# Optimization experiments

Hardware: AMD Instinct MI355X
Metric: run time of the kernel (lower is better)

The kernel has to match this reference:

```python
import jax, jax.numpy as jnp
import numpy as np

HEADS = 16
DIM_HEAD = 64
ROT_DIM = 32  # RotaryEmbedding(dim=dim_head//2) -> rotates first 32 channels
SCALE = DIM_HEAD ** -0.5


def _rope(x):
    # x: [b, h, n, d]; rotate first ROT_DIM channels, interleaved pairs (lucidrains style)
    n = x.shape[2]
    inv_freq = 1.0 / (10000.0 ** (jnp.arange(0, ROT_DIM, 2, dtype=jnp.float32) / ROT_DIM))  # [16]
    ang = jnp.arange(n, dtype=jnp.float32)[:, None] * inv_freq[None, :]  # [n, 16]
    cos, sin = jnp.cos(ang), jnp.sin(ang)  # [n, 16]
    x_rot, x_pass = x[..., :ROT_DIM], x[..., ROT_DIM:]
    x1 = x_rot[..., 0::2]  # [b,h,n,16]
    x2 = x_rot[..., 1::2]
    y1 = x1 * cos - x2 * sin
    y2 = x2 * cos + x1 * sin
    y = jnp.stack([y1, y2], axis=-1).reshape(x_rot.shape)  # re-interleave
    return jnp.concatenate([y, x_pass], axis=-1)


def setup_inputs() -> dict:
    key = jax.random.key(0)
    ks = jax.random.split(key, 5)
    b, n, d = 4, 2048, 1024
    inner = HEADS * DIM_HEAD
    return {
        "queries": jax.random.normal(ks[0], (b, n, d), jnp.float32),
        "Wq": jax.random.normal(ks[1], (d, inner), jnp.float32) * (d ** -0.5),
        "Wkv": jax.random.normal(ks[2], (d, 2 * inner), jnp.float32) * (d ** -0.5),
        "Wout": jax.random.normal(ks[3], (inner, d), jnp.float32) * (inner ** -0.5),
        "bout": jnp.zeros((d,), jnp.float32),
    }


def reference(queries, Wq, Wkv, Wout, bout):
    b, n, _ = queries.shape
    q = queries @ Wq                      # [b,n,inner]
    kv = queries @ Wkv                    # self-attention: context = queries
    k, v = jnp.split(kv, 2, axis=-1)
    split_heads = lambda t: t.reshape(b, n, HEADS, DIM_HEAD).transpose(0, 2, 1, 3)
    q, k, v = split_heads(q), split_heads(k), split_heads(v)
    q, k = _rope(q), _rope(k)
    sim = jnp.einsum('bhid,bhjd->bhij', q, k) * SCALE
    attn = jax.nn.softmax(sim, axis=-1)
    out = jnp.einsum('bhij,bhjd->bhid', attn, v)
    out = out.transpose(0, 2, 1, 3).reshape(b, n, HEADS * DIM_HEAD)
    return out @ Wout + bout
```

## Files before the change

### kernel.cpp

```cpp
#include <hip/hip_runtime.h>
#include <math.h>

#define BB    4
#define NN    2048
#define DD    1024
#define HH    16
#define DHD   64
#define INNER 1024
#define LOG2_10K_D16 0.8304820237218406f
#define SCALE_LOG2E 0.1803368801111601f

typedef short bf16x8 __attribute__((ext_vector_type(8)));
typedef short bf16x4 __attribute__((ext_vector_type(4)));
typedef float f32x4  __attribute__((ext_vector_type(4)));
typedef unsigned short u16x8 __attribute__((ext_vector_type(8)));

#define ASYNC16(g, l) __builtin_amdgcn_global_load_lds( \
    (const __attribute__((address_space(1))) void*)(g),  \
    (__attribute__((address_space(3))) void*)(l), 16, 0, 0)

#define MFMA16(a, b, c) __builtin_amdgcn_mfma_f32_16x16x32_bf16((a), (b), (c), 0, 0, 0)

static __device__ __forceinline__ float fexp2(float x) {
#if __has_builtin(__builtin_amdgcn_exp2f)
    return __builtin_amdgcn_exp2f(x);
#else
    float r;
    asm("v_exp_f32 %0, %1" : "=v"(r) : "v"(x));
    return r;
#endif
}

static __device__ __forceinline__ unsigned short f2bf(float f) {
    union { float f; unsigned int u; } v; v.f = f;
    unsigned int u = v.u;
    u += 0x7fffu + ((u >> 16) & 1u);
    return (unsigned short)(u >> 16);
}
static __device__ __forceinline__ unsigned int packbf2(float lo, float hi) {
    union { float f; unsigned int u; } a, b;
    a.f = lo; b.f = hi;
    return __builtin_amdgcn_perm(b.u + 0x8000u, a.u + 0x8000u, 0x07060302u);
}

__global__ __launch_bounds__(256) void cast_x_kernel(
    const float* __restrict__ X, unsigned short* __restrict__ Xb)
{
    const size_t i = ((size_t)blockIdx.x * 256 + threadIdx.x) * 8;
    const float4 a = *(const float4*)(X + i);
    const float4 b = *(const float4*)(X + i + 4);
    u16x8 o;
    o[0] = f2bf(a.x); o[1] = f2bf(a.y); o[2] = f2bf(a.z); o[3] = f2bf(a.w);
    o[4] = f2bf(b.x); o[5] = f2bf(b.y); o[6] = f2bf(b.z); o[7] = f2bf(b.w);
    *(u16x8*)(Xb + i) = o;
}

__global__ __launch_bounds__(256) void tcast_kernel(
    const float* __restrict__ src, unsigned short* __restrict__ dst,
    int K, int N)
{
    __shared__ float ts[32][33];
    const int t = threadIdx.x;
    const int n0 = blockIdx.x * 32, k0 = blockIdx.y * 32;
    const int r = t >> 5, c = t & 31;
    #pragma unroll
    for (int p = 0; p < 4; ++p)
        ts[r + p * 8][c] = src[(size_t)(k0 + r + p * 8) * N + n0 + c];
    __syncthreads();
    #pragma unroll
    for (int p = 0; p < 4; ++p)
        dst[(size_t)(n0 + r + p * 8) * K + k0 + c] = f2bf(ts[c][r + p * 8]);
}

__global__ __launch_bounds__(256) void proj_qkv_mfma(
    const unsigned short* __restrict__ Xb, const unsigned short* __restrict__ Wt,
    unsigned short* __restrict__ qb, unsigned short* __restrict__ kb,
    unsigned short* __restrict__ vb)
{
    __shared__ __align__(16) unsigned short As[128 * 32];
    __shared__ __align__(16) unsigned short Bs[128 * 32];

    const int t     = threadIdx.x;
    const int w     = t >> 6, lane = t & 63;
    const int lane4 = lane & 15, quad = lane >> 4, quad8 = quad * 8;
    const int wm    = w >> 1, wn = w & 1;
    const int m0    = blockIdx.y * 128, n0 = blockIdx.x * 128;

    const int srow = t >> 2, scol = (t & 3) * 8;
    const unsigned short* gA = Xb + (size_t)(m0 + srow) * DD + scol;
    const unsigned short* gB = Wt + (size_t)(n0 + srow) * DD + scol;
    unsigned short* lA = As + t * 8;
    unsigned short* lB = Bs + t * 8;

    f32x4 acc[4][4] = {};

    for (int k0 = 0; k0 < DD; k0 += 32) {
        __syncthreads();
        ASYNC16(gA + k0,            lA);
        ASYNC16(gA + 64 * DD + k0,  lA + 2048);
        ASYNC16(gB + k0,            lB);
        ASYNC16(gB + 64 * DD + k0,  lB + 2048);
        __syncthreads();

        bf16x8 a[4], b[4];
        #pragma unroll
        for (int i = 0; i < 4; ++i)
            a[i] = *(const bf16x8*)&As[(wm * 64 + i * 16 + lane4) * 32 + quad8];
        #pragma unroll
        for (int j = 0; j < 4; ++j)
            b[j] = *(const bf16x8*)&Bs[(wn * 64 + j * 16 + lane4) * 32 + quad8];
        #pragma unroll
        for (int i = 0; i < 4; ++i)
            #pragma unroll
            for (int j = 0; j < 4; ++j)
                acc[i][j] = MFMA16(a[i], b[j], acc[i][j]);
    }

    const int sec = n0 >> 10;

    if (sec == 2) {
        #pragma unroll
        for (int j = 0; j < 4; ++j) {
            const int csec = (n0 & 1023) + wn * 64 + j * 16;
            const int h    = csec >> 6;
            const int dh   = (csec & 63) + lane4;
            #pragma unroll
            for (int i = 0; i < 4; ++i) {
                const int rg0 = m0 + wm * 64 + i * 16 + quad * 4;
                const int b   = rg0 >> 11;
                const int n   = rg0 & 2047;
                uint2 pk;
                pk.x = packbf2(acc[i][j][0], acc[i][j][1]);
                pk.y = packbf2(acc[i][j][2], acc[i][j][3]);
                *(uint2*)(vb + (((size_t)b * HH + h) * DHD + dh) * NN + n) = pk;
            }
        }
    } else {
        unsigned short* dst = (sec == 0) ? qb : kb;
        const float qscale = (sec == 0) ? SCALE_LOG2E : 1.0f;
        #pragma unroll
        for (int j = 0; j < 4; ++j) {
            const int csec = (n0 & 1023) + wn * 64 + j * 16;
            const int h    = csec >> 6;
            const int dhb  = csec & 63;
            const int dh   = dhb + lane4;
            const bool rope = (dhb < 32);
            const float invf = fexp2(-(float)(dh >> 1) * LOG2_10K_D16);
            #pragma unroll
            for (int i = 0; i < 4; ++i) {
                #pragma unroll
                for (int r = 0; r < 4; ++r) {
                    const int rg = m0 + wm * 64 + i * 16 + quad * 4 + r;
                    const int b  = rg >> 11;
                    const int n  = rg & 2047;
                    float x = acc[i][j][r] * qscale;
                    if (rope) {
                        const float ang = (float)n * invf;
                        float s_, c_;
                        __sincosf(ang, &s_, &c_);
                        const float p = __shfl_xor(x, 1);
                        x = (lane4 & 1) ? fmaf(p, s_, x * c_)
                                        : fmaf(p, -s_, x * c_);
                    }
                    dst[(((size_t)b * HH + h) * NN + n) * DHD + dh] = f2bf(x);
                }
            }
        }
    }
}

__global__ __launch_bounds__(256, 2) void attn_kernel(
    const unsigned short* __restrict__ qb, const unsigned short* __restrict__ kb,
    const unsigned short* __restrict__ vtb, unsigned short* __restrict__ aob)
{
    __shared__ __align__(16) unsigned char smem[65536];
    unsigned short (*ks)[128][64] = (unsigned short (*)[128][64])smem;
    unsigned short (*vs)[64][128] = (unsigned short (*)[64][128])(smem + 32768);

    const int t     = threadIdx.x;
    const int kq    = t >> 6;
    const int lane  = t & 63;
    const int lane4 = lane & 15;
    const int quad  = lane >> 4;
    const int quad8 = quad * 8;
    const int l7    = lane4 & 7;

    const int bid = blockIdx.x;
    const int bh  = bid & 63;
    const int q0  = (bid >> 6) * 64;
    const size_t hb = (size_t)bh * NN * DHD;

    bf16x8 qf[4][2];
    #pragma unroll
    for (int qt = 0; qt < 4; ++qt) {
        const unsigned short* qrow = qb + hb + (size_t)(q0 + qt * 16 + lane4) * DHD;
        qf[qt][0] = *(const bf16x8*)(qrow + quad8);
        qf[qt][1] = *(const bf16x8*)(qrow + 32 + quad8);
    }

    bf16x8 onesf;
    #pragma unroll
    for (int j = 0; j < 8; ++j) onesf[j] = (short)0x3F80;

    const int krow0 = t >> 3;
    const int kcol  = ((t & 7) ^ (krow0 & 7)) * 8;
    const unsigned short* kg = kb + hb + (size_t)krow0 * DHD + (t & 7) * 8;
    const int vrow0 = t >> 4;
    const int vm    = t & 15;
    const int vr7   = vrow0 & 7;
    const int vcX   = (vm >> 1) & 3;
    const int vsub  = vm >> 3;
    const int vqA   = (2 * vm) & 3;
    const int vqB   = (2 * vm + 1) & 3;
    const int colA  = (((vcX * 4 + vqA) ^ vr7) * 8) + vsub * 4;
    const int colB  = (((vcX * 4 + vqB) ^ vr7) * 8) + vsub * 4;
    const unsigned short* vg = vtb + hb + (size_t)vrow0 * NN + vm * 8;

    f32x4 o[4][4], lacc[4];
    #pragma unroll
    for (int d = 0; d < 4; ++d)
        #pragma unroll
        for (int qt = 0; qt < 4; ++qt) o[d][qt] = (f32x4){0.f, 0.f, 0.f, 0.f};
    #pragma unroll
    for (int qt = 0; qt < 4; ++qt) lacc[qt] = (f32x4){0.f, 0.f, 0.f, 0.f};

    {
        bf16x8 kv[4], vv[4];
        #pragma unroll
        for (int s = 0; s < 4; ++s) {
            kv[s] = *(const bf16x8*)(kg + (size_t)s * 32 * DHD);
            vv[s] = *(const bf16x8*)(vg + (size_t)s * 16 * NN);
        }
        #pragma unroll
        for (int s = 0; s < 4; ++s) {
            *(bf16x8*)&ks[0][krow0 + 32 * s][kcol] = kv[s];
            bf16x4 lo = __builtin_shufflevector(vv[s], vv[s], 0, 1, 2, 3);
            bf16x4 hi = __builtin_shufflevector(vv[s], vv[s], 4, 5, 6, 7);
            *(bf16x4*)&vs[0][vrow0 + 16 * s][colA] = lo;
            *(bf16x4*)&vs[0][vrow0 + 16 * s][colB] = hi;
        }
    }
    __syncthreads();

    for (int kt = 0; kt < NN / 128; ++kt) {
        const int cur = kt & 1;
        const bool more = (kt + 1 < NN / 128);

        bf16x8 kv[4], vv[4];
        if (more) {
            #pragma unroll
            for (int s = 0; s < 4; ++s) {
                kv[s] = *(const bf16x8*)(kg + (size_t)(kt + 1) * 128 * DHD + (size_t)s * 32 * DHD);
                vv[s] = *(const bf16x8*)(vg + (kt + 1) * 128 + (size_t)s * 16 * NN);
            }
        }

        bf16x8 ak[2][2];
        #pragma unroll
        for (int sub = 0; sub < 2; ++sub) {
            const int row = sub * 64 + kq * 16 + lane4;
            ak[sub][0] = *(const bf16x8*)&ks[cur][row][(quad ^ l7) * 8];
            ak[sub][1] = *(const bf16x8*)&ks[cur][row][((quad + 4) ^ l7) * 8];
        }

        bf16x8 pb[4];
        #pragma unroll
        for (int qt = 0; qt < 4; ++qt) {
            f32x4 z0 = (f32x4){0.f, 0.f, 0.f, 0.f};
            f32x4 z1 = (f32x4){0.f, 0.f, 0.f, 0.f};
            z0 = MFMA16(ak[0][0], qf[qt][0], z0);
            z0 = MFMA16(ak[0][1], qf[qt][1], z0);
            z1 = MFMA16(ak[1][0], qf[qt][0], z1);
            z1 = MFMA16(ak[1][1], qf[qt][1], z1);
            union { unsigned int u[4]; bf16x8 v; } pk;
            pk.u[0] = packbf2(fexp2(z0[0]), fexp2(z0[1]));
            pk.u[1] = packbf2(fexp2(z0[2]), fexp2(z0[3]));
            pk.u[2] = packbf2(fexp2(z1[0]), fexp2(z1[1]));
            pk.u[3] = packbf2(fexp2(z1[2]), fexp2(z1[3]));
            pb[qt] = pk.v;
            lacc[qt] = MFMA16(onesf, pb[qt], lacc[qt]);
        }

        #pragma unroll
        for (int d = 0; d < 4; ++d) {
            const bf16x8 av = *(const bf16x8*)&vs[cur][d * 16 + lane4][((kq * 4 + quad) ^ l7) * 8];
            #pragma unroll
            for (int qt = 0; qt < 4; ++qt)
                o[d][qt] = MFMA16(av, pb[qt], o[d][qt]);
        }

        if (more) {
            #pragma unroll
            for (int s = 0; s < 4; ++s) {
                *(bf16x8*)&ks[cur ^ 1][krow0 + 32 * s][kcol] = kv[s];
                bf16x4 lo = __builtin_shufflevector(vv[s], vv[s], 0, 1, 2, 3);
                bf16x4 hi = __builtin_shufflevector(vv[s], vv[s], 4, 5, 6, 7);
                *(bf16x4*)&vs[cur ^ 1][vrow0 + 16 * s][colA] = lo;
                *(bf16x4*)&vs[cur ^ 1][vrow0 + 16 * s][colB] = hi;
            }
        }
        __syncthreads();
    }

    float* pbuf = (float*)smem;
    #pragma unroll
    for (int d = 0; d < 4; ++d)
        #pragma unroll
        for (int qt = 0; qt < 4; ++qt)
            #pragma unroll
            for (int r = 0; r < 4; ++r)
                pbuf[(kq * 64 + d * 16 + quad * 4 + r) * 64 + qt * 16 + lane4] = o[d][qt][r];
    __syncthreads();

    f32x4 of[4];
    #pragma unroll
    for (int d = 0; d < 4; ++d)
        #pragma unroll
        for (int r = 0; r < 4; ++r) {
            const int dh = d * 16 + quad * 4 + r;
            const int qc = kq * 16 + lane4;
            of[d][r] = pbuf[dh * 64 + qc] + pbuf[(64 + dh) * 64 + qc]
                     + pbuf[(128 + dh) * 64 + qc] + pbuf[(192 + dh) * 64 + qc];
        }
    __syncthreads();

    if (quad == 0) {
        #pragma unroll
        for (int qt = 0; qt < 4; ++qt)
            pbuf[(kq * 4 + qt) * 16 + lane4] = lacc[qt][0];
    }
    __syncthreads();
    const float lt = pbuf[(0 * 4 + kq) * 16 + lane4] + pbuf[(1 * 4 + kq) * 16 + lane4]
                   + pbuf[(2 * 4 + kq) * 16 + lane4] + pbuf[(3 * 4 + kq) * 16 + lane4];
    const float linv = 1.0f / lt;

    const int b = bh >> 4, h = bh & 15;
    const int n = q0 + kq * 16 + lane4;
    unsigned short* obase = aob + ((size_t)b * NN + n) * INNER + h * DHD;
    #pragma unroll
    for (int d = 0; d < 4; ++d) {
        uint2 pk;
        pk.x = packbf2(of[d][0] * linv, of[d][1] * linv);
        pk.y = packbf2(of[d][2] * linv, of[d][3] * linv);
        *(uint2*)(obase + d * 16 + quad * 4) = pk;
    }
}

__global__ __launch_bounds__(256) void out_proj_mfma(
    const unsigned short* __restrict__ Ab, const unsigned short* __restrict__ Wt,
    const float* __restrict__ bias, float* __restrict__ C)
{
    __shared__ __align__(16) unsigned short As[128 * 32];
    __shared__ __align__(16) unsigned short Bs[128 * 32];

    const int t     = threadIdx.x;
    const int w     = t >> 6, lane = t & 63;
    const int lane4 = lane & 15, quad = lane >> 4, quad8 = quad * 8;
    const int wm    = w >> 1, wn = w & 1;
    const int m0    = blockIdx.y * 128, n0 = blockIdx.x * 128;

    const int srow = t >> 2, scol = (t & 3) * 8;
    const unsigned short* gA = Ab + (size_t)(m0 + srow) * INNER + scol;
    const unsigned short* gB = Wt + (size_t)(n0 + srow) * INNER + scol;
    unsigned short* lA = As + t * 8;
    unsigned short* lB = Bs + t * 8;

    f32x4 acc[4][4] = {};

    for (int k0 = 0; k0 < INNER; k0 += 32) {
        __syncthreads();
        ASYNC16(gA + k0,               lA);
        ASYNC16(gA + 64 * INNER + k0,  lA + 2048);
        ASYNC16(gB + k0,               lB);
        ASYNC16(gB + 64 * INNER + k0,  lB + 2048);
        __syncthreads();

        bf16x8 a[4], b[4];
        #pragma unroll
        for (int i = 0; i < 4; ++i)
            a[i] = *(const bf16x8*)&As[(wm * 64 + i * 16 + lane4) * 32 + quad8];
        #pragma unroll
        for (int j = 0; j < 4; ++j)
            b[j] = *(const bf16x8*)&Bs[(wn * 64 + j * 16 + lane4) * 32 + quad8];
        #pragma unroll
        for (int i = 0; i < 4; ++i)
            #pragma unroll
            for (int j = 0; j < 4; ++j)
                acc[i][j] = MFMA16(a[i], b[j], acc[i][j]);
    }

    #pragma unroll
    for (int j = 0; j < 4; ++j) {
        const int col = n0 + wn * 64 + j * 16 + lane4;
        const float bv = bias[col];
        #pragma unroll
        for (int i = 0; i < 4; ++i)
            #pragma unroll
            for (int r = 0; r < 4; ++r) {
                const int rg = m0 + wm * 64 + i * 16 + quad * 4 + r;
                C[(size_t)rg * DD + col] = acc[i][j][r] + bv;
            }
    }
}

extern "C" void kernel_launch(void* const* d_in, const int* in_sizes, int n_in,
                              void* d_out, int out_size, void* d_ws, size_t ws_size,
                              hipStream_t stream)
{
    const float* X    = (const float*)d_in[0];
    const float* Wq   = (const float*)d_in[1];
    const float* Wkv  = (const float*)d_in[2];
    const float* Wout = (const float*)d_in[3];
    const float* bout = (const float*)d_in[4];
    float* out = (float*)d_out;

    const size_t E = (size_t)BB * HH * NN * DHD;
    unsigned short* qb  = (unsigned short*)d_ws;
    unsigned short* kb  = qb + E;
    unsigned short* vtb = kb + E;
    unsigned short* xb  = vtb + E;
    unsigned short* wt  = xb + E;
    unsigned short* wo  = wt + (size_t)3072 * 1024;

    cast_x_kernel<<<4096, 256, 0, stream>>>(X, xb);
    tcast_kernel<<<dim3(32, 32), 256, 0, stream>>>(Wq,   wt,               1024, 1024);
    tcast_kernel<<<dim3(64, 32), 256, 0, stream>>>(Wkv,  wt + 1024 * 1024, 1024, 2048);
    tcast_kernel<<<dim3(32, 32), 256, 0, stream>>>(Wout, wo,               1024, 1024);

    proj_qkv_mfma<<<dim3(3072 / 128, 8192 / 128), 256, 0, stream>>>(
        xb, wt, qb, kb, vtb);

    attn_kernel<<<dim3(NN / 64 * BB * HH), 256, 0, stream>>>(qb, kb, vtb, xb);

    out_proj_mfma<<<dim3(1024 / 128, 8192 / 128), 256, 0, stream>>>(
        xb, wo, bout, out);
}
```

Before: 299.2 us.

## Make K/V LDS tiles wave-private and drop per-iteration block barriers

Remaps the global-to-LDS loading of K and V so each wave writes exactly the K rows and V column slices it later reads for its own kq slice. With no cross-wave sharing of the staged tiles, the per-iteration __syncthreads in the key loop is removed, and only one barrier is kept before the shared reduction buffer is reused. The aim is to let waves drift independently and overlap memory and MFMA work instead of stalling at a barrier every tile. The risk is a correctness hazard if any LDS element is read by a wave other than the one that wrote it, and the changed access pattern may alter global coalescing or LDS bank conflicts.

```diff
diff --git a/kernel.cpp b/kernel.cpp
--- a/kernel.cpp
+++ b/kernel.cpp
@@ -202,18 +202,16 @@
     #pragma unroll
     for (int j = 0; j < 8; ++j) onesf[j] = (short)0x3F80;
 
-    const int krow0 = t >> 3;
-    const int kcol  = ((t & 7) ^ (krow0 & 7)) * 8;
-    const unsigned short* kg = kb + hb + (size_t)krow0 * DHD + (t & 7) * 8;
-    const int vrow0 = t >> 4;
-    const int vm    = t & 15;
+    const int krow  = kq * 16 + (lane >> 3);
+    const int kslot = ((lane & 7) ^ (lane >> 3)) * 8;
+    const unsigned short* kg = kb + hb + (size_t)krow * DHD + (lane & 7) * 8;
+
+    const int vrow0 = lane >> 2;
+    const int vm    = 2 * kq + (lane & 1) + ((lane >> 1) & 1) * 8;
     const int vr7   = vrow0 & 7;
-    const int vcX   = (vm >> 1) & 3;
-    const int vsub  = vm >> 3;
-    const int vqA   = (2 * vm) & 3;
-    const int vqB   = (2 * vm + 1) & 3;
-    const int colA  = (((vcX * 4 + vqA) ^ vr7) * 8) + vsub * 4;
-    const int colB  = (((vcX * 4 + vqB) ^ vr7) * 8) + vsub * 4;
+    const int halfo = (vm >> 3) * 4;
+    const int colA  = ((((vm & 7) * 2)     ^ vr7) * 8) + halfo;
+    const int colB  = ((((vm & 7) * 2 + 1) ^ vr7) * 8) + halfo;
     const unsigned short* vg = vtb + hb + (size_t)vrow0 * NN + vm * 8;
 
     f32x4 o[4][4], lacc[4];
@@ -225,34 +223,44 @@
     for (int qt = 0; qt < 4; ++qt) lacc[qt] = (f32x4){0.f, 0.f, 0.f, 0.f};
 
     {
-        bf16x8 kv[4], vv[4];
+        const bf16x8 k0 = *(const bf16x8*)(kg);
+        const bf16x8 k1 = *(const bf16x8*)(kg + 8 * DHD);
+        const bf16x8 k2 = *(const bf16x8*)(kg + 64 * DHD);
+        const bf16x8 k3 = *(const bf16x8*)(kg + 72 * DHD);
+        const bf16x8 v0 = *(const bf16x8*)(vg);
+        const bf16x8 v1 = *(const bf16x8*)(vg + (size_t)16 * NN);
+        const bf16x8 v2 = *(const bf16x8*)(vg + (size_t)32 * NN);
+        const bf16x8 v3 = *(const bf16x8*)(vg + (size_t)48 * NN);
+        *(bf16x8*)&ks[0][krow][kslot]      = k0;
+        *(bf16x8*)&ks[0][krow + 8][kslot]  = k1;
+        *(bf16x8*)&ks[0][krow + 64][kslot] = k2;
+        *(bf16x8*)&ks[0][krow + 72][kslot] = k3;
         #pragma unroll
         for (int s = 0; s < 4; ++s) {
-            kv[s] = *(const bf16x8*)(kg + (size_t)s * 32 * DHD);
-            vv[s] = *(const bf16x8*)(vg + (size_t)s * 16 * NN);
-        }
-        #pragma unroll
-        for (int s = 0; s < 4; ++s) {
-            *(bf16x8*)&ks[0][krow0 + 32 * s][kcol] = kv[s];
-            bf16x4 lo = __builtin_shufflevector(vv[s], vv[s], 0, 1, 2, 3);
-            bf16x4 hi = __builtin_shufflevector(vv[s], vv[s], 4, 5, 6, 7);
+            const bf16x8 vv = (s == 0) ? v0 : (s == 1) ? v1 : (s == 2) ? v2 : v3;
+            bf16x4 lo = __builtin_shufflevector(vv, vv, 0, 1, 2, 3);
+            bf16x4 hi = __builtin_shufflevector(vv, vv, 4, 5, 6, 7);
             *(bf16x4*)&vs[0][vrow0 + 16 * s][colA] = lo;
             *(bf16x4*)&vs[0][vrow0 + 16 * s][colB] = hi;
         }
     }
-    __syncthreads();
 
     for (int kt = 0; kt < NN / 128; ++kt) {
         const int cur = kt & 1;
         const bool more = (kt + 1 < NN / 128);
 
-        bf16x8 kv[4], vv[4];
+        bf16x8 nk0, nk1, nk2, nk3, nv0, nv1, nv2, nv3;
         if (more) {
-            #pragma unroll
-            for (int s = 0; s < 4; ++s) {
-                kv[s] = *(const bf16x8*)(kg + (size_t)(kt + 1) * 128 * DHD + (size_t)s * 32 * DHD);
-                vv[s] = *(const bf16x8*)(vg + (kt + 1) * 128 + (size_t)s * 16 * NN);
-            }
+            const unsigned short* kgn = kg + (size_t)(kt + 1) * 128 * DHD;
+            const unsigned short* vgn = vg + (kt + 1) * 128;
+            nk0 = *(const bf16x8*)(kgn);
+            nk1 = *(const bf16x8*)(kgn + 8 * DHD);
+            nk2 = *(const bf16x8*)(kgn + 64 * DHD);
+            nk3 = *(const bf16x8*)(kgn + 72 * DHD);
+            nv0 = *(const bf16x8*)(vgn);
+            nv1 = *(const bf16x8*)(vgn + (size_t)16 * NN);
+            nv2 = *(const bf16x8*)(vgn + (size_t)32 * NN);
+            nv3 = *(const bf16x8*)(vgn + (size_t)48 * NN);
         }
 
         bf16x8 ak[2][2];
@@ -290,18 +298,23 @@
         }
 
         if (more) {
+            const int nb = cur ^ 1;
+            *(bf16x8*)&ks[nb][krow][kslot]      = nk0;
+            *(bf16x8*)&ks[nb][krow + 8][kslot]  = nk1;
+            *(bf16x8*)&ks[nb][krow + 64][kslot] = nk2;
+            *(bf16x8*)&ks[nb][krow + 72][kslot] = nk3;
             #pragma unroll
             for (int s = 0; s < 4; ++s) {
-                *(bf16x8*)&ks[cur ^ 1][krow0 + 32 * s][kcol] = kv[s];
-                bf16x4 lo = __builtin_shufflevector(vv[s], vv[s], 0, 1, 2, 3);
-                bf16x4 hi = __builtin_shufflevector(vv[s], vv[s], 4, 5, 6, 7);
-                *(bf16x4*)&vs[cur ^ 1][vrow0 + 16 * s][colA] = lo;
-                *(bf16x4*)&vs[cur ^ 1][vrow0 + 16 * s][colB] = hi;
+                const bf16x8 vv = (s == 0) ? nv0 : (s == 1) ? nv1 : (s == 2) ? nv2 : nv3;
+                bf16x4 lo = __builtin_shufflevector(vv, vv, 0, 1, 2, 3);
+                bf16x4 hi = __builtin_shufflevector(vv, vv, 4, 5, 6, 7);
+                *(bf16x4*)&vs[nb][vrow0 + 16 * s][colA] = lo;
+                *(bf16x4*)&vs[nb][vrow0 + 16 * s][colB] = hi;
             }
         }
-        __syncthreads();
-    }
-
+    }
+
+    __syncthreads();
     float* pbuf = (float*)smem;
     #pragma unroll
     for (int d = 0; d < 4; ++d)
```

New measurement: 312.2 us. +4.4%, slower.

## Load K/V fragments directly from global into registers, drop LDS staging

Applied to the files above, without the earlier changes.

The attention kernel no longer stages K and V tiles through shared memory with barriers. Each wave now loads its own MFMA fragments straight from global memory into registers, double-buffered across two register sets. The row-sum is computed with scalar adds plus cross-lane shuffles instead of a ones-vector MFMA. This removes LDS writes and reads and the per-tile __syncthreads, but each wave now fetches its fragments on its own with narrower, less coalesced loads. It also raises register pressure under the 2-blocks-per-CU launch bound.

```diff
diff --git a/kernel.cpp b/kernel.cpp
--- a/kernel.cpp
+++ b/kernel.cpp
@@ -174,8 +174,6 @@
     const unsigned short* __restrict__ vtb, unsigned short* __restrict__ aob)
 {
     __shared__ __align__(16) unsigned char smem[65536];
-    unsigned short (*ks)[128][64] = (unsigned short (*)[128][64])smem;
-    unsigned short (*vs)[64][128] = (unsigned short (*)[64][128])(smem + 32768);
 
     const int t     = threadIdx.x;
     const int kq    = t >> 6;
@@ -183,7 +181,6 @@
     const int lane4 = lane & 15;
     const int quad  = lane >> 4;
     const int quad8 = quad * 8;
-    const int l7    = lane4 & 7;
 
     const int bid = blockIdx.x;
     const int bh  = bid & 63;
@@ -198,108 +195,91 @@
         qf[qt][1] = *(const bf16x8*)(qrow + 32 + quad8);
     }
 
-    bf16x8 onesf;
-    #pragma unroll
-    for (int j = 0; j < 8; ++j) onesf[j] = (short)0x3F80;
-
-    const int krow0 = t >> 3;
-    const int kcol  = ((t & 7) ^ (krow0 & 7)) * 8;
-    const unsigned short* kg = kb + hb + (size_t)krow0 * DHD + (t & 7) * 8;
-    const int vrow0 = t >> 4;
-    const int vm    = t & 15;
-    const int vr7   = vrow0 & 7;
-    const int vcX   = (vm >> 1) & 3;
-    const int vsub  = vm >> 3;
-    const int vqA   = (2 * vm) & 3;
-    const int vqB   = (2 * vm + 1) & 3;
-    const int colA  = (((vcX * 4 + vqA) ^ vr7) * 8) + vsub * 4;
-    const int colB  = (((vcX * 4 + vqB) ^ vr7) * 8) + vsub * 4;
-    const unsigned short* vg = vtb + hb + (size_t)vrow0 * NN + vm * 8;
-
-    f32x4 o[4][4], lacc[4];
+    const unsigned short* kfb = kb + hb + (size_t)(kq * 16 + lane4) * DHD + quad8;
+    const unsigned short* vflo = vtb + hb + (size_t)lane4 * NN + kq * 16 + quad * 4;
+    const unsigned short* vfhi = vflo + 64;
+
+    f32x4 o[4][4];
+    float lsum[4] = {0.f, 0.f, 0.f, 0.f};
     #pragma unroll
     for (int d = 0; d < 4; ++d)
         #pragma unroll
         for (int qt = 0; qt < 4; ++qt) o[d][qt] = (f32x4){0.f, 0.f, 0.f, 0.f};
-    #pragma unroll
-    for (int qt = 0; qt < 4; ++qt) lacc[qt] = (f32x4){0.f, 0.f, 0.f, 0.f};
-
-    {
-        bf16x8 kv[4], vv[4];
-        #pragma unroll
-        for (int s = 0; s < 4; ++s) {
-            kv[s] = *(const bf16x8*)(kg + (size_t)s * 32 * DHD);
-            vv[s] = *(const bf16x8*)(vg + (size_t)s * 16 * NN);
+
+    bf16x8 akA[2][2], akB[2][2];
+    bf16x4 avloA[4], avhiA[4], avloB[4], avhiB[4];
+
+#define LOADK(dst, kt) do {                                                      \
+    dst[0][0] = *(const bf16x8*)(kfb + (size_t)((kt) * 128)      * DHD);         \
+    dst[0][1] = *(const bf16x8*)(kfb + (size_t)((kt) * 128)      * DHD + 32);    \
+    dst[1][0] = *(const bf16x8*)(kfb + (size_t)((kt) * 128 + 64) * DHD);         \
+    dst[1][1] = *(const bf16x8*)(kfb + (size_t)((kt) * 128 + 64) * DHD + 32);    \
+} while (0)
+
+#define LOADV(dlo, dhi, kt) do {                                                 \
+    _Pragma("unroll")                                                            \
+    for (int d_ = 0; d_ < 4; ++d_) {                                             \
+        dlo[d_] = *(const bf16x4*)(vflo + (size_t)d_ * 16 * NN + (kt) * 128);    \
+        dhi[d_] = *(const bf16x4*)(vfhi + (size_t)d_ * 16 * NN + (kt) * 128);    \
+    }                                                                            \
+} while (0)
+
+#define COMPUTE(ak, avlo, avhi) do {                                             \
+    bf16x8 pb_[4];                                                               \
+    _Pragma("unroll")                                                            \
+    for (int qt_ = 0; qt_ < 4; ++qt_) {                                          \
+        f32x4 z0 = (f32x4){0.f, 0.f, 0.f, 0.f};                                  \
+        f32x4 z1 = (f32x4){0.f, 0.f, 0.f, 0.f};                                  \
+        z0 = MFMA16(ak[0][0], qf[qt_][0], z0);                                   \
+        z0 = MFMA16(ak[0][1], qf[qt_][1], z0);                                   \
+        z1 = MFMA16(ak[1][0], qf[qt_][0], z1);                                   \
+        z1 = MFMA16(ak[1][1], qf[qt_][1], z1);                                   \
+        const float e00 = fexp2(z0[0]), e01 = fexp2(z0[1]);                      \
+        const float e02 = fexp2(z0[2]), e03 = fexp2(z0[3]);                      \
+        const float e10 = fexp2(z1[0]), e11 = fexp2(z1[1]);                      \
+        const float e12 = fexp2(z1[2]), e13 = fexp2(z1[3]);                      \
+        union { unsigned int u[4]; bf16x8 v; } pk_;                              \
+        pk_.u[0] = packbf2(e00, e01);                                            \
+        pk_.u[1] = packbf2(e02, e03);                                            \
+        pk_.u[2] = packbf2(e10, e11);                                            \
+        pk_.u[3] = packbf2(e12, e13);                                            \
+        pb_[qt_] = pk_.v;                                                        \
+        lsum[qt_] += ((e00 + e01) + (e02 + e03)) + ((e10 + e11) + (e12 + e13));  \
+    }                                                                            \
+    _Pragma("unroll")                                                            \
+    for (int d_ = 0; d_ < 4; ++d_) {                                             \
+        const bf16x8 av_ = __builtin_shufflevector(avlo[d_], avhi[d_],           \
+                                                   0, 1, 2, 3, 4, 5, 6, 7);      \
+        _Pragma("unroll")                                                        \
+        for (int qt_ = 0; qt_ < 4; ++qt_)                                        \
+            o[d_][qt_] = MFMA16(av_, pb_[qt_], o[d_][qt_]);                      \
+    }                                                                            \
+} while (0)
+
+    LOADK(akA, 0);
+    LOADV(avloA, avhiA, 0);
+
+    for (int kt = 0; kt < NN / 128; kt += 2) {
+        LOADK(akB, kt + 1);
+        LOADV(avloB, avhiB, kt + 1);
+        COMPUTE(akA, avloA, avhiA);
+        if (kt + 2 < NN / 128) {
+            LOADK(akA, kt + 2);
+            LOADV(avloA, avhiA, kt + 2);
         }
-        #pragma unroll
-        for (int s = 0; s < 4; ++s) {
-            *(bf16x8*)&ks[0][krow0 + 32 * s][kcol] = kv[s];
-            bf16x4 lo = __builtin_shufflevector(vv[s], vv[s], 0, 1, 2, 3);
-            bf16x4 hi = __builtin_shufflevector(vv[s], vv[s], 4, 5, 6, 7);
-            *(bf16x4*)&vs[0][vrow0 + 16 * s][colA] = lo;
-            *(bf16x4*)&vs[0][vrow0 + 16 * s][colB] = hi;
-        }
-    }
-    __syncthreads();
-
-    for (int kt = 0; kt < NN / 128; ++kt) {
-        const int cur = kt & 1;
-        const bool more = (kt + 1 < NN / 128);
-
-        bf16x8 kv[4], vv[4];
-        if (more) {
-            #pragma unroll
-            for (int s = 0; s < 4; ++s) {
-                kv[s] = *(const bf16x8*)(kg + (size_t)(kt + 1) * 128 * DHD + (size_t)s * 32 * DHD);
-                vv[s] = *(const bf16x8*)(vg + (kt + 1) * 128 + (size_t)s * 16 * NN);
-            }
-        }
-
-        bf16x8 ak[2][2];
-        #pragma unroll
-        for (int sub = 0; sub < 2; ++sub) {
-            const int row = sub * 64 + kq * 16 + lane4;
-            ak[sub][0] = *(const bf16x8*)&ks[cur][row][(quad ^ l7) * 8];
-            ak[sub][1] = *(const bf16x8*)&ks[cur][row][((quad + 4) ^ l7) * 8];
-        }
-
-        bf16x8 pb[4];
-        #pragma unroll
-        for (int qt = 0; qt < 4; ++qt) {
-            f32x4 z0 = (f32x4){0.f, 0.f, 0.f, 0.f};
-            f32x4 z1 = (f32x4){0.f, 0.f, 0.f, 0.f};
-            z0 = MFMA16(ak[0][0], qf[qt][0], z0);
-            z0 = MFMA16(ak[0][1], qf[qt][1], z0);
-            z1 = MFMA16(ak[1][0], qf[qt][0], z1);
-            z1 = MFMA16(ak[1][1], qf[qt][1], z1);
-            union { unsigned int u[4]; bf16x8 v; } pk;
-            pk.u[0] = packbf2(fexp2(z0[0]), fexp2(z0[1]));
-            pk.u[1] = packbf2(fexp2(z0[2]), fexp2(z0[3]));
-            pk.u[2] = packbf2(fexp2(z1[0]), fexp2(z1[1]));
-            pk.u[3] = packbf2(fexp2(z1[2]), fexp2(z1[3]));
-            pb[qt] = pk.v;
-            lacc[qt] = MFMA16(onesf, pb[qt], lacc[qt]);
-        }
-
-        #pragma unroll
-        for (int d = 0; d < 4; ++d) {
-            const bf16x8 av = *(const bf16x8*)&vs[cur][d * 16 + lane4][((kq * 4 + quad) ^ l7) * 8];
-            #pragma unroll
-            for (int qt = 0; qt < 4; ++qt)
-                o[d][qt] = MFMA16(av, pb[qt], o[d][qt]);
-        }
-
-        if (more) {
-            #pragma unroll
-            for (int s = 0; s < 4; ++s) {
-                *(bf16x8*)&ks[cur ^ 1][krow0 + 32 * s][kcol] = kv[s];
-                bf16x4 lo = __builtin_shufflevector(vv[s], vv[s], 0, 1, 2, 3);
-                bf16x4 hi = __builtin_shufflevector(vv[s], vv[s], 4, 5, 6, 7);
-                *(bf16x4*)&vs[cur ^ 1][vrow0 + 16 * s][colA] = lo;
-                *(bf16x4*)&vs[cur ^ 1][vrow0 + 16 * s][colB] = hi;
-            }
-        }
-        __syncthreads();
+        COMPUTE(akB, avloB, avhiB);
+    }
+
+#undef LOADK
+#undef LOADV
+#undef COMPUTE
+
+    #pragma unroll
+    for (int qt = 0; qt < 4; ++qt) {
+        float v = lsum[qt];
+        v += __shfl_xor(v, 16);
+        v += __shfl_xor(v, 32);
+        lsum[qt] = v;
     }
 
     float* pbuf = (float*)smem;
@@ -327,7 +307,7 @@
     if (quad == 0) {
         #pragma unroll
         for (int qt = 0; qt < 4; ++qt)
-            pbuf[(kq * 4 + qt) * 16 + lane4] = lacc[qt][0];
+            pbuf[(kq * 4 + qt) * 16 + lane4] = lsum[qt];
     }
     __syncthreads();
     const float lt = pbuf[(0 * 4 + kq) * 16 + lane4] + pbuf[(1 * 4 + kq) * 16 + lane4]
```

Result: slower. 383.3 us (+28.1%).
